# Kernel optimization log

Measured on AMD Instinct MI355X. Metric: run time of the kernel, lower is better.

The kernel has to match this reference:

```python
import jax, jax.numpy as jnp
import numpy as np

N = 50000      # nodes
E = 800000     # edges (before self-loops)
DIN = 128      # input feature dim
DOUT = 128     # per-head output dim
H = 4          # heads (concat=False -> mean over heads)
SLOPE = 0.2    # PyG GATConv default negative_slope


def setup_inputs() -> dict:
    key = jax.random.key(0)
    k1, k2, k3, k4, k5 = jax.random.split(key, 5)
    x = jax.random.normal(k1, (N, DIN), dtype=jnp.float32)
    edge_index = jax.random.randint(k2, (2, E), 0, N)
    W = jax.random.normal(k3, (DIN, H * DOUT), dtype=jnp.float32) / np.sqrt(DIN).astype(np.float32)
    att_src = jax.random.normal(k4, (H, DOUT), dtype=jnp.float32) * 0.1
    att_dst = jax.random.normal(k5, (H, DOUT), dtype=jnp.float32) * 0.1
    return {"x": x, "edge_index": edge_index, "W": W, "att_src": att_src, "att_dst": att_dst}


def _gat(x, W, att_src, att_dst, src, dst):
    h = (x @ W).reshape(N, H, DOUT)                      # [N,H,C] shared lin for src/dst
    a_s = jnp.einsum('nhc,hc->nh', h, att_src)           # [N,H]
    a_d = jnp.einsum('nhc,hc->nh', h, att_dst)           # [N,H]
    logits = jax.nn.leaky_relu(a_s[src] + a_d[dst], SLOPE)   # [Etot,H]
    m = jax.ops.segment_max(logits, dst, num_segments=N)     # segment softmax (stable)
    e = jnp.exp(logits - m[dst])
    denom = jax.ops.segment_sum(e, dst, num_segments=N)
    alpha = e / (denom[dst] + 1e-16)                         # [Etot,H]
    out = jax.ops.segment_sum(alpha[:, :, None] * h[src], dst, num_segments=N)  # [N,H,C]
    return out.mean(axis=1)                                   # concat=False -> average heads


def reference(x, edge_index, W, att_src, att_dst):
    loop = jnp.arange(N, dtype=edge_index.dtype)          # add_self_loops=True (PyG default)
    src = jnp.concatenate([edge_index[0], loop])
    dst = jnp.concatenate([edge_index[1], loop])
    return _gat(x, W, att_src, att_dst, src, dst)
```

## Files before the change

kernel.cpp:

```cpp
#include <hip/hip_runtime.h>

#define NN 50000
#define EE 800000
#define ETOT (EE + NN)
#define MAXD 64
#define NBK 196
#define CAP 6144
#define CHX 2304
#define TM 16

typedef _Float16 f16x8 __attribute__((ext_vector_type(8)));
typedef _Float16 f16x2 __attribute__((ext_vector_type(2)));
typedef float f32x4 __attribute__((ext_vector_type(4)));
typedef float f32x2 __attribute__((ext_vector_type(2)));
typedef unsigned int u32x4 __attribute__((ext_vector_type(4)));

__device__ __forceinline__ float lrelu(float v) { return v > 0.f ? v : 0.2f * v; }
__device__ __forceinline__ unsigned int pack2(float a, float b) {
  unsigned short lo = __builtin_bit_cast(unsigned short, (_Float16)a);
  unsigned short hi = __builtin_bit_cast(unsigned short, (_Float16)b);
  return (unsigned int)lo | ((unsigned int)hi << 16);
}

__global__ void k_prep(const float* __restrict__ W,
                       const float* __restrict__ att_s,
                       const float* __restrict__ att_d,
                       unsigned short* __restrict__ Bt,
                       float* __restrict__ WaS, float* __restrict__ WaD,
                       int* __restrict__ bcnt) {
  int gid = blockIdx.x * blockDim.x + threadIdx.x;
  if (gid < NBK) bcnt[gid] = 0;
  if (gid < 128 * 512) {
    int col = gid >> 9, k = gid & 511;
    float v = W[(k & 127) * 512 + (k >> 7) * 128 + col];
    _Float16 hv = (_Float16)v;
    Bt[col * 512 + k] = __builtin_bit_cast(unsigned short, hv);
  }
  if (gid < 512) {
    int k = gid >> 2, h = gid & 3;
    const float* wrow = W + k * 512 + h * 128;
    const float* as = att_s + h * 128;
    const float* ad = att_d + h * 128;
    float ss = 0.f, sd = 0.f;
    for (int c = 0; c < 128; ++c) { float w = wrow[c]; ss += w * as[c]; sd += w * ad[c]; }
    WaS[k * 4 + h] = ss;
    WaD[k * 4 + h] = sd;
  }
}

__global__ __launch_bounds__(256) void k_xcast_p1(const float* __restrict__ x,
                                                  const float* __restrict__ WaS,
                                                  const float* __restrict__ WaD,
                                                  const int* __restrict__ ei,
                                                  unsigned int* __restrict__ xh,
                                                  float* __restrict__ a_s,
                                                  float* __restrict__ a_d,
                                                  int* __restrict__ bcnt,
                                                  unsigned int* __restrict__ ebuf) {
  __shared__ unsigned long long D[128][33];
  __shared__ float4 wsl[128];
  __shared__ float4 wdl[128];
  __shared__ int cnt[NBK];
  __shared__ int gbase[NBK];
  int t = threadIdx.x;
  int nb = blockIdx.x * 128;
  if (t < 128) wsl[t] = ((const float4*)WaS)[t];
  else wdl[t - 128] = ((const float4*)WaD)[t - 128];
  for (int i = t; i < NBK; i += 256) cnt[i] = 0;

#pragma unroll
  for (int i = 0; i < 16; ++i) {
    int idx = t + i * 256;
    int n = idx >> 5, c4 = idx & 31;
    int gn = nb + n;
    float4 v = make_float4(0.f, 0.f, 0.f, 0.f);
    if (gn < NN) v = ((const float4*)x)[(size_t)gn * 32 + c4];
    unsigned int lo = pack2(v.x, v.y);
    unsigned int hi = pack2(v.z, v.w);
    if (gn < NN) ((uint2*)xh)[(size_t)gn * 32 + c4] = make_uint2(lo, hi);
    D[n][c4] = (unsigned long long)lo | ((unsigned long long)hi << 32);
  }
  __syncthreads();

  {
    int n = t >> 1, half = t & 1;
    float s0 = 0.f, s1 = 0.f, s2 = 0.f, s3 = 0.f;
    float d0 = 0.f, d1 = 0.f, d2 = 0.f, d3 = 0.f;
#pragma unroll
    for (int p = 0; p < 16; ++p) {
      int c4 = 2 * p + half;
      unsigned long long q = D[n][c4];
      f16x2 lo2 = __builtin_bit_cast(f16x2, (unsigned int)q);
      f16x2 hi2 = __builtin_bit_cast(f16x2, (unsigned int)(q >> 32));
      float f0 = (float)lo2[0], f1 = (float)lo2[1];
      float f2 = (float)hi2[0], f3 = (float)hi2[1];
      int c = c4 * 4;
      float4 w0 = wsl[c], w1 = wsl[c + 1], w2 = wsl[c + 2], w3 = wsl[c + 3];
      s0 += f0 * w0.x + f1 * w1.x + f2 * w2.x + f3 * w3.x;
      s1 += f0 * w0.y + f1 * w1.y + f2 * w2.y + f3 * w3.y;
      s2 += f0 * w0.z + f1 * w1.z + f2 * w2.z + f3 * w3.z;
      s3 += f0 * w0.w + f1 * w1.w + f2 * w2.w + f3 * w3.w;
      float4 v0 = wdl[c], v1 = wdl[c + 1], v2 = wdl[c + 2], v3 = wdl[c + 3];
      d0 += f0 * v0.x + f1 * v1.x + f2 * v2.x + f3 * v3.x;
      d1 += f0 * v0.y + f1 * v1.y + f2 * v2.y + f3 * v3.y;
      d2 += f0 * v0.z + f1 * v1.z + f2 * v2.z + f3 * v3.z;
      d3 += f0 * v0.w + f1 * v1.w + f2 * v2.w + f3 * v3.w;
    }
    s0 += __shfl_xor(s0, 1); s1 += __shfl_xor(s1, 1);
    s2 += __shfl_xor(s2, 1); s3 += __shfl_xor(s3, 1);
    d0 += __shfl_xor(d0, 1); d1 += __shfl_xor(d1, 1);
    d2 += __shfl_xor(d2, 1); d3 += __shfl_xor(d3, 1);
    int gn = nb + n;
    if (half == 0 && gn < NN) {
      *(float4*)(a_s + gn * 4) = make_float4(s0, s1, s2, s3);
      *(float4*)(a_d + gn * 4) = make_float4(d0, d1, d2, d3);
    }
  }

  int e0 = blockIdx.x * CHX;
#pragma unroll
  for (int k = 0; k < CHX / 256; ++k) {
    int e = e0 + t + k * 256;
    if (e < ETOT) {
      int d = (e < EE) ? ei[EE + e] : (e - EE);
      atomicAdd(&cnt[d >> 8], 1);
    }
  }
  __syncthreads();
  for (int i = t; i < NBK; i += 256) {
    gbase[i] = (cnt[i] > 0) ? atomicAdd(&bcnt[i], cnt[i]) : 0;
    cnt[i] = 0;
  }
  __syncthreads();
#pragma unroll
  for (int k = 0; k < CHX / 256; ++k) {
    int e = e0 + t + k * 256;
    if (e < ETOT) {
      int s, d;
      if (e < EE) { s = ei[e]; d = ei[EE + e]; } else { s = d = e - EE; }
      int b = d >> 8;
      int idx = gbase[b] + atomicAdd(&cnt[b], 1);
      if (idx < CAP)
        ebuf[(size_t)b * CAP + idx] = (unsigned int)s | ((unsigned int)(d & 255) << 16);
    }
  }
}

__global__ __launch_bounds__(256) void k_p2(const unsigned int* __restrict__ ebuf,
                                            const int* __restrict__ bcnt,
                                            int* __restrict__ rs,
                                            unsigned short* __restrict__ perm16) {
  __shared__ int sb[256];
  __shared__ int loc[256];
  __shared__ int cnt[256];
  __shared__ unsigned short out16[CAP];
  __shared__ int basesh;
  int b = blockIdx.x, t = threadIdx.x;

  int v = (t < NBK) ? bcnt[t] : 0;
  sb[t] = v;
  __syncthreads();
  for (int off = 1; off < 256; off <<= 1) {
    int u = (t >= off) ? sb[t - off] : 0;
    __syncthreads();
    sb[t] += u;
    __syncthreads();
  }
  if (t == b) basesh = sb[t] - v;
  cnt[t] = 0;
  __syncthreads();

  int base = basesh;
  int m = min(bcnt[b], CAP);
  int d0 = b * 256;
  const unsigned int* rec = ebuf + (size_t)b * CAP;
  for (int i = t; i < m; i += 256) atomicAdd(&cnt[rec[i] >> 16], 1);
  __syncthreads();

  int c = cnt[t];
  sb[t] = c;
  __syncthreads();
  for (int off = 1; off < 256; off <<= 1) {
    int u = (t >= off) ? sb[t - off] : 0;
    __syncthreads();
    sb[t] += u;
    __syncthreads();
  }
  int ex = sb[t] - c;
  loc[t] = ex;
  int gi = d0 + t;
  if (gi < NN) rs[gi] = base + ex;
  if (b == NBK - 1 && t == 0) rs[NN] = base + m;
  cnt[t] = 0;
  __syncthreads();

  for (int i = t; i < m; i += 256) {
    unsigned int r = rec[i];
    int dl = r >> 16;
    int rk = atomicAdd(&cnt[dl], 1);
    out16[loc[dl] + rk] = (unsigned short)(r & 0xffffu);
  }
  __syncthreads();
  for (int i = t; i < m; i += 256) perm16[base + i] = out16[i];
}

__global__ __launch_bounds__(1024, 2) void k_fused(const float* __restrict__ a_s,
                                                   const float* __restrict__ a_d,
                                                   const unsigned int* __restrict__ xh,
                                                   const int* __restrict__ rs,
                                                   const unsigned short* __restrict__ perm16,
                                                   const unsigned short* __restrict__ Bt,
                                                   float* __restrict__ out) {
  __shared__ u32x4 Zl[TM * 64];
  __shared__ f32x2 wlo[16][MAXD];
  __shared__ f32x2 whi[16][MAXD];
  __shared__ unsigned short sn_s[16][MAXD];
  unsigned int* Zw = (unsigned int*)Zl;
  int wave = threadIdx.x >> 6, lane = threadIdx.x & 63;
  int m0 = blockIdx.x * TM;
  int n = m0 + wave;

  int s = rs[n];
  int deg = rs[n + 1] - s;
  float4 ad = *(const float4*)(a_d + n * 4);
  bool fast = (deg <= MAXD);

  float t0 = 0.f, t1 = 0.f, t2 = 0.f, t3 = 0.f;
  if (fast) {
    if (lane < deg) {
      int sn = perm16[s + lane];
      sn_s[wave][lane] = (unsigned short)sn;
      float4 as = *(const float4*)(a_s + sn * 4);
      float e0 = __expf(lrelu(as.x + ad.x));
      float e1 = __expf(lrelu(as.y + ad.y));
      float e2 = __expf(lrelu(as.z + ad.z));
      float e3 = __expf(lrelu(as.w + ad.w));
      wlo[wave][lane] = (f32x2){e0, e1};
      whi[wave][lane] = (f32x2){e2, e3};
      t0 = e0; t1 = e1; t2 = e2; t3 = e3;
    }
  } else {
    for (int j = lane; j < deg; j += 64) {
      int sn = perm16[s + j];
      float4 as = *(const float4*)(a_s + sn * 4);
      t0 += __expf(lrelu(as.x + ad.x)); t1 += __expf(lrelu(as.y + ad.y));
      t2 += __expf(lrelu(as.z + ad.z)); t3 += __expf(lrelu(as.w + ad.w));
    }
  }
#pragma unroll
  for (int off = 32; off; off >>= 1) {
    t0 += __shfl_xor(t0, off); t1 += __shfl_xor(t1, off);
    t2 += __shfl_xor(t2, off); t3 += __shfl_xor(t3, off);
  }
  float sc0 = 0.25f / (t0 + 1e-16f), sc1 = 0.25f / (t1 + 1e-16f);
  float sc2 = 0.25f / (t2 + 1e-16f), sc3 = 0.25f / (t3 + 1e-16f);
  __builtin_amdgcn_wave_barrier();

  f32x2 za0 = {0.f, 0.f}, za1 = {0.f, 0.f}, za2 = {0.f, 0.f}, za3 = {0.f, 0.f};
  if (fast) {
    int j = 0;
    for (; j + 8 <= deg; j += 8) {
      unsigned int u[8];
#pragma unroll
      for (int k = 0; k < 8; ++k) u[k] = xh[(int)sn_s[wave][j + k] * 64 + lane];
#pragma unroll
      for (int k = 0; k < 8; ++k) {
        f32x2 wl = wlo[wave][j + k];
        f32x2 wh = whi[wave][j + k];
        f16x2 p = __builtin_bit_cast(f16x2, u[k]);
        f32x2 xv = {(float)p[0], (float)p[1]};
        za0 += wl[0] * xv; za1 += wl[1] * xv;
        za2 += wh[0] * xv; za3 += wh[1] * xv;
      }
    }
    if (j + 4 <= deg) {
      unsigned int u[4];
#pragma unroll
      for (int k = 0; k < 4; ++k) u[k] = xh[(int)sn_s[wave][j + k] * 64 + lane];
#pragma unroll
      for (int k = 0; k < 4; ++k) {
        f32x2 wl = wlo[wave][j + k];
        f32x2 wh = whi[wave][j + k];
        f16x2 p = __builtin_bit_cast(f16x2, u[k]);
        f32x2 xv = {(float)p[0], (float)p[1]};
        za0 += wl[0] * xv; za1 += wl[1] * xv;
        za2 += wh[0] * xv; za3 += wh[1] * xv;
      }
      j += 4;
    }
    for (; j < deg; ++j) {
      f32x2 wl = wlo[wave][j];
      f32x2 wh = whi[wave][j];
      unsigned int u = xh[(int)sn_s[wave][j] * 64 + lane];
      f16x2 p = __builtin_bit_cast(f16x2, u);
      f32x2 xv = {(float)p[0], (float)p[1]};
      za0 += wl[0] * xv; za1 += wl[1] * xv;
      za2 += wh[0] * xv; za3 += wh[1] * xv;
    }
  } else {
    for (int j = 0; j < deg; ++j) {
      int sn = perm16[s + j];
      float4 as = *(const float4*)(a_s + sn * 4);
      float w0 = __expf(lrelu(as.x + ad.x));
      float w1 = __expf(lrelu(as.y + ad.y));
      float w2 = __expf(lrelu(as.z + ad.z));
      float w3 = __expf(lrelu(as.w + ad.w));
      unsigned int u = xh[sn * 64 + lane];
      f16x2 p = __builtin_bit_cast(f16x2, u);
      f32x2 xv = {(float)p[0], (float)p[1]};
      za0 += w0 * xv; za1 += w1 * xv; za2 += w2 * xv; za3 += w3 * xv;
    }
  }

  unsigned int pk0 = pack2(za0[0] * sc0, za0[1] * sc0);
  unsigned int pk1 = pack2(za1[0] * sc1, za1[1] * sc1);
  unsigned int pk2 = pack2(za2[0] * sc2, za2[1] * sc2);
  unsigned int pk3 = pack2(za3[0] * sc3, za3[1] * sc3);
  int rb = wave & 7;
  int ct = lane >> 2, sub = lane & 3;
  Zw[wave * 256 + (((0 * 16 + ct) ^ rb) << 2) + sub] = pk0;
  Zw[wave * 256 + (((1 * 16 + ct) ^ rb) << 2) + sub] = pk1;
  Zw[wave * 256 + (((2 * 16 + ct) ^ rb) << 2) + sub] = pk2;
  Zw[wave * 256 + (((3 * 16 + ct) ^ rb) << 2) + sub] = pk3;
  __syncthreads();

  if (wave >= 8) return;

  int lr = lane & 15, lk = lane >> 4;
  int n0w = wave * 16;
  const u32x4* Bv = (const u32x4*)Bt;
  f32x4 acc = (f32x4){0.f, 0.f, 0.f, 0.f};
#pragma unroll
  for (int kk = 0; kk < 16; ++kk) {
    f16x8 af = __builtin_bit_cast(f16x8, Zl[lr * 64 + ((kk * 4 + lk) ^ (lr & 7))]);
    f16x8 bf = __builtin_bit_cast(f16x8, Bv[(n0w + lr) * 64 + kk * 4 + lk]);
    acc = __builtin_amdgcn_mfma_f32_16x16x32_f16(af, bf, acc, 0, 0, 0);
  }
  int cr = lk * 4;
#pragma unroll
  for (int j2 = 0; j2 < 4; ++j2) {
    out[(m0 + cr + j2) * 128 + n0w + lr] = acc[j2];
  }
}

extern "C" void kernel_launch(void* const* d_in, const int* in_sizes, int n_in,
                              void* d_out, int out_size, void* d_ws, size_t ws_size,
                              hipStream_t stream) {
  const float* x = (const float*)d_in[0];
  const int* ei = (const int*)d_in[1];
  const float* W = (const float*)d_in[2];
  const float* att_s = (const float*)d_in[3];
  const float* att_d = (const float*)d_in[4];
  float* out = (float*)d_out;
  char* ws = (char*)d_ws;

  unsigned int* xh = (unsigned int*)(ws + 0);
  unsigned int* ebuf = (unsigned int*)(ws + 12800000);
  unsigned short* Bt = (unsigned short*)(ws + 17616896);
  float* WaS = (float*)(ws + 17747968);
  float* WaD = (float*)(ws + 17750016);
  float* a_s = (float*)(ws + 17752064);
  float* a_d = (float*)(ws + 18552064);
  int* rs = (int*)(ws + 19352064);
  int* bcnt = (int*)(ws + 19552256);
  unsigned short* perm16 = (unsigned short*)(ws + 19553280);

  k_prep<<<256, 256, 0, stream>>>(W, att_s, att_d, Bt, WaS, WaD, bcnt);
  k_xcast_p1<<<(NN + 127) / 128, 256, 0, stream>>>(x, WaS, WaD, ei, xh, a_s, a_d, bcnt, ebuf);
  k_p2<<<NBK, 256, 0, stream>>>(ebuf, bcnt, rs, perm16);
  k_fused<<<NN / TM, 1024, 0, stream>>>(a_s, a_d, xh, rs, perm16, Bt, out);
}
```

Before: 139.0 us.

## Split fused aggregate+GEMM kernel into separate aggregation and tiled MFMA GEMM kernels

The single fused kernel, where 1024-thread blocks aggregated 16 nodes and half the waves ran a small MFMA GEMM, is split in two. The first kernel aggregates each node into per-head fp16 z vectors in a global buffer, using 256-thread blocks and byte-offset gather addressing. The second is a 64-row tiled MFMA GEMM that stages A and B through swizzled LDS. This aims to improve occupancy and GEMM reuse of B, at the cost of an extra launch and a round-trip of roughly 51 MB of z data through global memory.

```diff
diff --git a/kernel.cpp b/kernel.cpp
--- a/kernel.cpp
+++ b/kernel.cpp
@@ -7,7 +7,6 @@
 #define NBK 196
 #define CAP 6144
 #define CHX 2304
-#define TM 16
 
 typedef _Float16 f16x8 __attribute__((ext_vector_type(8)));
 typedef _Float16 f16x2 __attribute__((ext_vector_type(2)));
@@ -204,39 +203,32 @@
   for (int i = t; i < m; i += 256) perm16[base + i] = out16[i];
 }
 
-__global__ __launch_bounds__(1024, 2) void k_fused(const float* __restrict__ a_s,
-                                                   const float* __restrict__ a_d,
-                                                   const unsigned int* __restrict__ xh,
-                                                   const int* __restrict__ rs,
-                                                   const unsigned short* __restrict__ perm16,
-                                                   const unsigned short* __restrict__ Bt,
-                                                   float* __restrict__ out) {
-  __shared__ u32x4 Zl[TM * 64];
-  __shared__ f32x2 wlo[16][MAXD];
-  __shared__ f32x2 whi[16][MAXD];
-  __shared__ unsigned short sn_s[16][MAXD];
-  unsigned int* Zw = (unsigned int*)Zl;
+__global__ __launch_bounds__(256) void k_aggz(const float* __restrict__ a_s,
+                                              const float* __restrict__ a_d,
+                                              const unsigned int* __restrict__ xh,
+                                              const int* __restrict__ rs,
+                                              const unsigned short* __restrict__ perm16,
+                                              unsigned int* __restrict__ zbuf) {
+  __shared__ unsigned int off_s[4][MAXD];
+  __shared__ float4 w_s[4][MAXD];
   int wave = threadIdx.x >> 6, lane = threadIdx.x & 63;
-  int m0 = blockIdx.x * TM;
-  int n = m0 + wave;
-
-  int s = rs[n];
-  int deg = rs[n + 1] - s;
+  int n = blockIdx.x * 4 + wave;
   float4 ad = *(const float4*)(a_d + n * 4);
+  int s = rs[n], e = rs[n + 1];
+  int deg = e - s;
   bool fast = (deg <= MAXD);
 
   float t0 = 0.f, t1 = 0.f, t2 = 0.f, t3 = 0.f;
   if (fast) {
     if (lane < deg) {
       int sn = perm16[s + lane];
-      sn_s[wave][lane] = (unsigned short)sn;
+      off_s[wave][lane] = (unsigned int)sn * 256u;
       float4 as = *(const float4*)(a_s + sn * 4);
       float e0 = __expf(lrelu(as.x + ad.x));
       float e1 = __expf(lrelu(as.y + ad.y));
       float e2 = __expf(lrelu(as.z + ad.z));
       float e3 = __expf(lrelu(as.w + ad.w));
-      wlo[wave][lane] = (f32x2){e0, e1};
-      whi[wave][lane] = (f32x2){e2, e3};
+      w_s[wave][lane] = make_float4(e0, e1, e2, e3);
       t0 = e0; t1 = e1; t2 = e2; t3 = e3;
     }
   } else {
@@ -256,46 +248,44 @@
   float sc2 = 0.25f / (t2 + 1e-16f), sc3 = 0.25f / (t3 + 1e-16f);
   __builtin_amdgcn_wave_barrier();
 
+  const char* xb = (const char*)xh;
+  int lb = lane * 4;
   f32x2 za0 = {0.f, 0.f}, za1 = {0.f, 0.f}, za2 = {0.f, 0.f}, za3 = {0.f, 0.f};
   if (fast) {
     int j = 0;
     for (; j + 8 <= deg; j += 8) {
       unsigned int u[8];
 #pragma unroll
-      for (int k = 0; k < 8; ++k) u[k] = xh[(int)sn_s[wave][j + k] * 64 + lane];
+      for (int k = 0; k < 8; ++k)
+        u[k] = *(const unsigned int*)(xb + off_s[wave][j + k] + lb);
 #pragma unroll
       for (int k = 0; k < 8; ++k) {
-        f32x2 wl = wlo[wave][j + k];
-        f32x2 wh = whi[wave][j + k];
+        float4 w = w_s[wave][j + k];
         f16x2 p = __builtin_bit_cast(f16x2, u[k]);
         f32x2 xv = {(float)p[0], (float)p[1]};
-        za0 += wl[0] * xv; za1 += wl[1] * xv;
-        za2 += wh[0] * xv; za3 += wh[1] * xv;
+        za0 += w.x * xv; za1 += w.y * xv; za2 += w.z * xv; za3 += w.w * xv;
       }
     }
     if (j + 4 <= deg) {
       unsigned int u[4];
 #pragma unroll
-      for (int k = 0; k < 4; ++k) u[k] = xh[(int)sn_s[wave][j + k] * 64 + lane];
+      for (int k = 0; k < 4; ++k)
+        u[k] = *(const unsigned int*)(xb + off_s[wave][j + k] + lb);
 #pragma unroll
       for (int k = 0; k < 4; ++k) {
-        f32x2 wl = wlo[wave][j + k];
-        f32x2 wh = whi[wave][j + k];
+        float4 w = w_s[wave][j + k];
         f16x2 p = __builtin_bit_cast(f16x2, u[k]);
         f32x2 xv = {(float)p[0], (float)p[1]};
-        za0 += wl[0] * xv; za1 += wl[1] * xv;
-        za2 += wh[0] * xv; za3 += wh[1] * xv;
+        za0 += w.x * xv; za1 += w.y * xv; za2 += w.z * xv; za3 += w.w * xv;
       }
       j += 4;
     }
     for (; j < deg; ++j) {
-      f32x2 wl = wlo[wave][j];
-      f32x2 wh = whi[wave][j];
-      unsigned int u = xh[(int)sn_s[wave][j] * 64 + lane];
+      float4 w = w_s[wave][j];
+      unsigned int u = *(const unsigned int*)(xb + off_s[wave][j] + lb);
       f16x2 p = __builtin_bit_cast(f16x2, u);
       f32x2 xv = {(float)p[0], (float)p[1]};
-      za0 += wl[0] * xv; za1 += wl[1] * xv;
-      za2 += wh[0] * xv; za3 += wh[1] * xv;
+      za0 += w.x * xv; za1 += w.y * xv; za2 += w.z * xv; za3 += w.w * xv;
     }
   } else {
     for (int j = 0; j < deg; ++j) {
@@ -312,34 +302,82 @@
     }
   }
 
-  unsigned int pk0 = pack2(za0[0] * sc0, za0[1] * sc0);
-  unsigned int pk1 = pack2(za1[0] * sc1, za1[1] * sc1);
-  unsigned int pk2 = pack2(za2[0] * sc2, za2[1] * sc2);
-  unsigned int pk3 = pack2(za3[0] * sc3, za3[1] * sc3);
-  int rb = wave & 7;
-  int ct = lane >> 2, sub = lane & 3;
-  Zw[wave * 256 + (((0 * 16 + ct) ^ rb) << 2) + sub] = pk0;
-  Zw[wave * 256 + (((1 * 16 + ct) ^ rb) << 2) + sub] = pk1;
-  Zw[wave * 256 + (((2 * 16 + ct) ^ rb) << 2) + sub] = pk2;
-  Zw[wave * 256 + (((3 * 16 + ct) ^ rb) << 2) + sub] = pk3;
-  __syncthreads();
-
-  if (wave >= 8) return;
-
+  zbuf[n * 256 + 0 * 64 + lane] = pack2(za0[0] * sc0, za0[1] * sc0);
+  zbuf[n * 256 + 1 * 64 + lane] = pack2(za1[0] * sc1, za1[1] * sc1);
+  zbuf[n * 256 + 2 * 64 + lane] = pack2(za2[0] * sc2, za2[1] * sc2);
+  zbuf[n * 256 + 3 * 64 + lane] = pack2(za3[0] * sc3, za3[1] * sc3);
+}
+
+__global__ __launch_bounds__(256) void k_gemmz(const unsigned short* __restrict__ zbuf,
+                                               const unsigned short* __restrict__ Bt,
+                                               float* __restrict__ out) {
+  __shared__ u32x4 Al[1024];
+  __shared__ u32x4 Bl[2048];
+  int m0 = blockIdx.x * 64;
+  int wave = threadIdx.x >> 6, lane = threadIdx.x & 63;
+  int wm = (wave >> 1) * 32, wn = (wave & 1) * 64;
   int lr = lane & 15, lk = lane >> 4;
-  int n0w = wave * 16;
-  const u32x4* Bv = (const u32x4*)Bt;
-  f32x4 acc = (f32x4){0.f, 0.f, 0.f, 0.f};
-#pragma unroll
-  for (int kk = 0; kk < 16; ++kk) {
-    f16x8 af = __builtin_bit_cast(f16x8, Zl[lr * 64 + ((kk * 4 + lk) ^ (lr & 7))]);
-    f16x8 bf = __builtin_bit_cast(f16x8, Bv[(n0w + lr) * 64 + kk * 4 + lk]);
-    acc = __builtin_amdgcn_mfma_f32_16x16x32_f16(af, bf, acc, 0, 0, 0);
-  }
+
+  f32x4 acc[2][4];
+#pragma unroll
+  for (int mi = 0; mi < 2; ++mi)
+#pragma unroll
+    for (int ni = 0; ni < 4; ++ni) acc[mi][ni] = (f32x4){0.f, 0.f, 0.f, 0.f};
+
+  for (int t = 0; t < 4; ++t) {
+#pragma unroll
+    for (int i = 0; i < 4; ++i) {
+      int id = threadIdx.x + 256 * i;
+      int row = id >> 4, kc = id & 15;
+      int grow = m0 + row;
+      u32x4 v = {0u, 0u, 0u, 0u};
+      if (grow < NN) v = *(const u32x4*)((const char*)zbuf + grow * 1024 + t * 256 + kc * 16);
+      Al[row * 16 + (kc ^ (row & 7))] = v;
+    }
+#pragma unroll
+    for (int i = 0; i < 8; ++i) {
+      int id = threadIdx.x + 256 * i;
+      int col = id >> 4, kc = id & 15;
+      u32x4 v = *(const u32x4*)((const char*)Bt + col * 1024 + t * 256 + kc * 16);
+      Bl[col * 16 + (kc ^ (col & 7))] = v;
+    }
+    __syncthreads();
+#pragma unroll
+    for (int ks = 0; ks < 4; ++ks) {
+      f16x8 af[2], bf[4];
+#pragma unroll
+      for (int mi = 0; mi < 2; ++mi) {
+        int r = wm + mi * 16 + lr;
+        af[mi] = __builtin_bit_cast(f16x8, Al[r * 16 + ((ks * 4 + lk) ^ (r & 7))]);
+      }
+#pragma unroll
+      for (int ni = 0; ni < 4; ++ni) {
+        int c = wn + ni * 16 + lr;
+        bf[ni] = __builtin_bit_cast(f16x8, Bl[c * 16 + ((ks * 4 + lk) ^ (c & 7))]);
+      }
+#pragma unroll
+      for (int mi = 0; mi < 2; ++mi)
+#pragma unroll
+        for (int ni = 0; ni < 4; ++ni)
+          acc[mi][ni] = __builtin_amdgcn_mfma_f32_16x16x32_f16(af[mi], bf[ni], acc[mi][ni], 0, 0, 0);
+    }
+    __syncthreads();
+  }
+
   int cr = lk * 4;
 #pragma unroll
-  for (int j2 = 0; j2 < 4; ++j2) {
-    out[(m0 + cr + j2) * 128 + n0w + lr] = acc[j2];
+  for (int mi = 0; mi < 2; ++mi) {
+#pragma unroll
+    for (int j = 0; j < 4; ++j) {
+      int row = m0 + wm + mi * 16 + cr + j;
+      if (row < NN) {
+#pragma unroll
+        for (int ni = 0; ni < 4; ++ni) {
+          int col = wn + ni * 16 + lr;
+          out[row * 128 + col] = acc[mi][ni][j];
+        }
+      }
+    }
   }
 }
 
@@ -355,18 +393,20 @@
   char* ws = (char*)d_ws;
 
   unsigned int* xh = (unsigned int*)(ws + 0);
+  unsigned int* zbuf = (unsigned int*)(ws + 12800000);
   unsigned int* ebuf = (unsigned int*)(ws + 12800000);
-  unsigned short* Bt = (unsigned short*)(ws + 17616896);
-  float* WaS = (float*)(ws + 17747968);
-  float* WaD = (float*)(ws + 17750016);
-  float* a_s = (float*)(ws + 17752064);
-  float* a_d = (float*)(ws + 18552064);
-  int* rs = (int*)(ws + 19352064);
-  int* bcnt = (int*)(ws + 19552256);
-  unsigned short* perm16 = (unsigned short*)(ws + 19553280);
+  unsigned short* Bt = (unsigned short*)(ws + 64000000);
+  float* WaS = (float*)(ws + 64131072);
+  float* WaD = (float*)(ws + 64133120);
+  float* a_s = (float*)(ws + 64135168);
+  float* a_d = (float*)(ws + 64935168);
+  int* rs = (int*)(ws + 65735168);
+  int* bcnt = (int*)(ws + 65935360);
+  unsigned short* perm16 = (unsigned short*)(ws + 65936384);
 
   k_prep<<<256, 256, 0, stream>>>(W, att_s, att_d, Bt, WaS, WaD, bcnt);
   k_xcast_p1<<<(NN + 127) / 128, 256, 0, stream>>>(x, WaS, WaD, ei, xh, a_s, a_d, bcnt, ebuf);
   k_p2<<<NBK, 256, 0, stream>>>(ebuf, bcnt, rs, perm16);
-  k_fused<<<NN / TM, 1024, 0, stream>>>(a_s, a_d, xh, rs, perm16, Bt, out);
-}
+  k_aggz<<<NN / 4, 256, 0, stream>>>(a_s, a_d, xh, rs, perm16, zbuf);
+  k_gemmz<<<(NN + 63) / 64, 256, 0, stream>>>((const unsigned short*)zbuf, Bt, out);
+}
```

After: 122.6 us. 11.7% less time.
